# Kernel tuning notes

Measured on AMD Instinct MI355X. Metric: run time of the kernel, lower is better.

## Reference

```python
import jax, jax.numpy as jnp
import numpy as np

BS, SEQ, D = 8, 2048, 128
MASK_VALUE = -1000000.0


def setup_inputs() -> dict:
    key = jax.random.key(0)
    kq, kk, kv, kl = jax.random.split(key, 4)
    return {
        "queries": jax.random.normal(kq, (BS, SEQ, D), dtype=jnp.float32),
        "keys": jax.random.normal(kk, (BS, SEQ, D), dtype=jnp.float32),
        "values": jax.random.normal(kv, (BS, SEQ, D), dtype=jnp.float32),
        "valid_lens": jax.random.randint(kl, (BS,), 1, SEQ + 1, dtype=jnp.int32),
    }


def reference(queries, keys, values, valid_lens):
    d_k = keys.shape[-1]
    # (bs, seq_q, seq_k)
    scores = jnp.einsum("bqd,bkd->bqk", queries, keys) / jnp.sqrt(
        jnp.asarray(d_k, dtype=queries.dtype)
    )
    # padding mask over the LAST axis: position k valid iff k < valid_len[b]
    pos = jnp.arange(scores.shape[-1])  # (seq_k,)
    valid = pos[None, None, :] < valid_lens[:, None, None]  # (bs, 1, seq_k)
    scores = jnp.where(valid, scores, MASK_VALUE)
    attn = jax.nn.softmax(scores, axis=-1)
    # (bs, seq_q, d_v); dropout=0.0 -> identity
    return jnp.einsum("bqk,bkd->bqd", attn, values)
```

## Files before the change

### kernel.cpp

```cpp
#include <hip/hip_runtime.h>

typedef float f32x4 __attribute__((ext_vector_type(4)));
typedef short bf16x8 __attribute__((ext_vector_type(8)));
typedef short bf16x4 __attribute__((ext_vector_type(4)));
typedef unsigned int u32x2 __attribute__((ext_vector_type(2)));

#define BS    8
#define SEQ   2048
#define DH    128
#define BQ    32
#define BK    64
#define NT    256
#define CFIX  8.0f
#define SC2E  0.12751743f
#define NC2E  -11.541560327f

__device__ __forceinline__ unsigned short f2bf(float x) {
    unsigned u = __float_as_uint(x);
    u += 0x7FFFu + ((u >> 16) & 1u);
    return (unsigned short)(u >> 16);
}

__device__ __forceinline__ void gl_lds16(const unsigned short* g, unsigned short* l) {
    __builtin_amdgcn_global_load_lds(
        (const __attribute__((address_space(1))) unsigned int*)g,
        (__attribute__((address_space(3))) unsigned int*)l, 16, 0, 0);
}

__global__ __launch_bounds__(NT)
void conv_all(const float* __restrict__ K, const float* __restrict__ V,
              unsigned short* __restrict__ Kbf, unsigned short* __restrict__ Vt) {
    __shared__ unsigned short T[64][132];
    const int tid = threadIdx.x;
    const int bid = blockIdx.x;

    const int gtid = bid * NT + tid;
    #pragma unroll
    for (int i = 0; i < 8; ++i) {
        const int idx = i * (256 * NT) + gtid;
        float4 v = ((const float4*)K)[idx];
        ushort4 h;
        h.x = f2bf(v.x); h.y = f2bf(v.y); h.z = f2bf(v.z); h.w = f2bf(v.w);
        ((ushort4*)Kbf)[idx] = h;
    }

    const int vb = bid >> 5, s0 = (bid & 31) * 64;
    const float* Vb = V + ((size_t)vb * SEQ + s0) * DH;
    #pragma unroll
    for (int i = 0; i < 8; ++i) {
        const int row = i * 8 + (tid >> 5);
        const int col = (tid & 31) * 4;
        float4 v = *(const float4*)(Vb + (size_t)row * DH + col);
        ushort4 h;
        h.x = f2bf(v.x); h.y = f2bf(v.y); h.z = f2bf(v.z); h.w = f2bf(v.w);
        *(ushort4*)&T[row][col] = h;
    }
    __syncthreads();
    const int d = tid >> 1, sh = (tid & 1) * 32;
    unsigned short tmp[32] __attribute__((aligned(16)));
    #pragma unroll
    for (int s = 0; s < 32; ++s) tmp[s] = T[sh + s][d];
    unsigned short* dst = Vt + ((size_t)vb * DH + d) * SEQ + s0 + sh;
    #pragma unroll
    for (int g = 0; g < 4; ++g)
        *(uint4*)(dst + g * 8) = *(const uint4*)(tmp + g * 8);
}

__global__ __launch_bounds__(NT, 2)
void attn32sk(const float* __restrict__ Q, const unsigned short* __restrict__ Kbf,
              const unsigned short* __restrict__ Vt, const int* __restrict__ vlens,
              float* __restrict__ Oh, float* __restrict__ Lh) {
    __shared__ unsigned short Ks[2][BK * DH];
    __shared__ unsigned short Vs[2][DH * BK];
    __shared__ float Lsc[2][32];

    const int tid  = threadIdx.x;
    const int wid  = tid >> 6, lane = tid & 63;
    const int quad = lane >> 4, l16 = lane & 15;
    const int qh   = wid >> 1, sh = wid & 1;
    const int bid  = blockIdx.x;
    const int h    = bid & 1;
    const int rest = bid >> 1;
    const int b    = rest >> 6;
    const int q0   = (rest & 63) * BQ;
    const int vl   = vlens[b];

    const int ntiles = (vl + BK - 1) >> 6;
    const int t0 = h << 4;
    const int t1 = min(ntiles, (h + 1) << 4);

    float* Lrow = Lh + ((size_t)h * BS + b) * SEQ + q0;
    if (t0 >= t1) {
        if (tid < BQ) Lrow[tid] = 0.0f;
        return;
    }

    const unsigned short* Kb  = Kbf + (size_t)b * SEQ * DH;
    const unsigned short* Vtb = Vt  + (size_t)b * DH * SEQ;

    bf16x8 qf[4];
    {
        const float* Qr = Q + ((size_t)b * SEQ + q0 + 16 * qh + l16) * DH;
        #pragma unroll
        for (int ks = 0; ks < 4; ++ks) {
            const float4 x = *(const float4*)(Qr + 32 * ks + 8 * quad);
            const float4 y = *(const float4*)(Qr + 32 * ks + 8 * quad + 4);
            unsigned short t8[8] __attribute__((aligned(16)));
            t8[0] = f2bf(x.x); t8[1] = f2bf(x.y); t8[2] = f2bf(x.z); t8[3] = f2bf(x.w);
            t8[4] = f2bf(y.x); t8[5] = f2bf(y.y); t8[6] = f2bf(y.z); t8[7] = f2bf(y.w);
            qf[ks] = *(const bf16x8*)t8;
        }
    }

    f32x4 o[8];
    #pragma unroll
    for (int n = 0; n < 8; ++n) o[n] = (f32x4){0.f, 0.f, 0.f, 0.f};
    float lsum = 0.f;

    auto stage = [&](int buf, int k0) {
        unsigned short* KsB = &Ks[buf][0];
        unsigned short* VsB = &Vs[buf][0];
        #pragma unroll
        for (int ii = 0; ii < 4; ++ii) {
            const int rb = 16 * wid + 4 * ii;
            const int r  = rb + (lane >> 4);
            const int c  = lane & 15;
            gl_lds16(Kb + (size_t)(k0 + r) * DH + ((c ^ (r & 15)) << 3),
                     KsB + (size_t)rb * DH);
        }
        #pragma unroll
        for (int jj = 0; jj < 4; ++jj) {
            const int db = 32 * wid + 8 * jj;
            const int d  = db + (lane >> 3);
            const int c  = lane & 7;
            gl_lds16(Vtb + (size_t)d * SEQ + k0 + ((c ^ (d & 7)) << 3),
                     VsB + (size_t)db * BK);
        }
    };

    stage(0, t0 << 6);

    for (int t = t0; t < t1; ++t) {
        const int k0 = t << 6;
        __syncthreads();
        if (t + 1 < t1) stage((t + 1) & 1, k0 + BK);

        const unsigned short* Kt  = &Ks[t & 1][0];
        const unsigned short* Vtl = &Vs[t & 1][0];

        f32x4 s2[2];
        s2[0] = (f32x4){0.f, 0.f, 0.f, 0.f};
        s2[1] = (f32x4){0.f, 0.f, 0.f, 0.f};
        __builtin_amdgcn_s_setprio(1);
        #pragma unroll
        for (int ks = 0; ks < 4; ++ks) {
            bf16x8 bk[2];
            #pragma unroll
            for (int nt = 0; nt < 2; ++nt)
                bk[nt] = *(const bf16x8*)(Kt + (size_t)(32 * sh + 16 * nt + l16) * DH +
                                          (((4 * ks + quad) ^ l16) << 3));
            #pragma unroll
            for (int nt = 0; nt < 2; ++nt)
                s2[nt] = __builtin_amdgcn_mfma_f32_16x16x32_bf16(bk[nt], qf[ks], s2[nt], 0, 0, 0);
        }
        __builtin_amdgcn_s_setprio(0);

        float p[2][4];
        if (k0 + BK <= vl) {
            #pragma unroll
            for (int nt = 0; nt < 2; ++nt)
                #pragma unroll
                for (int r = 0; r < 4; ++r) {
                    const float pv = __builtin_amdgcn_exp2f(fmaf(s2[nt][r], SC2E, NC2E));
                    p[nt][r] = pv;
                    lsum += pv;
                }
        } else {
            const int kb = k0 + 32 * sh + 4 * quad;
            #pragma unroll
            for (int nt = 0; nt < 2; ++nt)
                #pragma unroll
                for (int r = 0; r < 4; ++r) {
                    float pv = __builtin_amdgcn_exp2f(fmaf(s2[nt][r], SC2E, NC2E));
                    pv = (kb + 16 * nt + r < vl) ? pv : 0.0f;
                    p[nt][r] = pv;
                    lsum += pv;
                }
        }

        bf16x4 pa[2];
        #pragma unroll
        for (int nt = 0; nt < 2; ++nt) {
            unsigned w0, w1;
            asm("v_cvt_pk_bf16_f32 %0, %1, %2" : "=v"(w0) : "v"(p[nt][0]), "v"(p[nt][1]));
            asm("v_cvt_pk_bf16_f32 %0, %1, %2" : "=v"(w1) : "v"(p[nt][2]), "v"(p[nt][3]));
            u32x2 tw; tw.x = w0; tw.y = w1;
            pa[nt] = __builtin_bit_cast(bf16x4, tw);
        }

        __builtin_amdgcn_s_setprio(1);
        #pragma unroll
        for (int n = 0; n < 8; ++n) {
            const int dd = 16 * n + l16;
            #pragma unroll
            for (int nt = 0; nt < 2; ++nt) {
                const int g = 4 * sh + 2 * nt + (quad >> 1);
                const bf16x4 vb = *(const bf16x4*)(Vtl + (size_t)dd * BK +
                                        ((g ^ (dd & 7)) << 3) + ((quad & 1) << 2));
                o[n] = __builtin_amdgcn_mfma_f32_16x16x16bf16_1k(pa[nt], vb, o[n], 0, 0, 0);
            }
        }
        __builtin_amdgcn_s_setprio(0);
    }

    lsum += __shfl_xor(lsum, 16, 64);
    lsum += __shfl_xor(lsum, 32, 64);

    __syncthreads();
    float* Osc = (float*)&Ks[0][0];

    if (lane < 16) Lsc[sh][qh * 16 + l16] = lsum;
    if (sh == 0) {
        #pragma unroll
        for (int r = 0; r < 4; ++r) {
            float* dst = Osc + (size_t)qh * 2048 + (4 * quad + r) * 128 + l16;
            #pragma unroll
            for (int n = 0; n < 8; ++n) dst[16 * n] = o[n][r];
        }
    }
    __syncthreads();
    if (sh == 1) {
        #pragma unroll
        for (int r = 0; r < 4; ++r) {
            const int row = 16 * qh + 4 * quad + r;
            const float ls = Lsc[0][qh * 16 + 4 * quad + r] +
                             Lsc[1][qh * 16 + 4 * quad + r];
            const float* src = Osc + (size_t)qh * 2048 + (4 * quad + r) * 128 + l16;
            float* Or = Oh + (((size_t)h * BS + b) * SEQ + q0 + row) * DH + l16;
            #pragma unroll
            for (int n = 0; n < 8; ++n)
                Or[16 * n] = o[n][r] + src[16 * n];
            if (l16 == 0) Lrow[row] = ls;
        }
    }
}

__global__ __launch_bounds__(NT)
void combine(const float* __restrict__ Oh, const float* __restrict__ Lh,
             float* __restrict__ Out) {
    const int bid = blockIdx.x;
    const int tid = threadIdx.x;
    const int b = bid >> 6, q0 = (bid & 63) * BQ;
    const int row = q0 + (tid >> 3);
    const int c0 = (tid & 7) * 16;
    const size_t r0 = (size_t)b * SEQ + row;

    const float l0 = Lh[r0];
    const float l1 = Lh[(size_t)BS * SEQ + r0];
    const float inv = 1.0f / (l0 + l1);

    const float* p0 = Oh + r0 * DH + c0;
    const float* p1 = Oh + (size_t)BS * SEQ * DH + r0 * DH + c0;
    float* po = Out + r0 * DH + c0;

    if (l1 != 0.0f) {
        #pragma unroll
        for (int j = 0; j < 4; ++j) {
            f32x4 a = *(const f32x4*)(p0 + 4 * j) + *(const f32x4*)(p1 + 4 * j);
            float4 ov;
            ov.x = a[0] * inv; ov.y = a[1] * inv;
            ov.z = a[2] * inv; ov.w = a[3] * inv;
            *(float4*)(po + 4 * j) = ov;
        }
    } else {
        #pragma unroll
        for (int j = 0; j < 4; ++j) {
            const f32x4 a = *(const f32x4*)(p0 + 4 * j);
            float4 ov;
            ov.x = a[0] * inv; ov.y = a[1] * inv;
            ov.z = a[2] * inv; ov.w = a[3] * inv;
            *(float4*)(po + 4 * j) = ov;
        }
    }
}

#define FBQ 32
#define QSTRIDE (DH + 4)
#define PSTRIDE (BK + 4)
__global__ __launch_bounds__(NT, 2)
void attn_fwd(const float* __restrict__ Q, const float* __restrict__ K,
              const float* __restrict__ V, const int* __restrict__ vlens,
              float* __restrict__ Out) {
    __shared__ float Qs[FBQ][QSTRIDE];
    __shared__ float KVs[BK][QSTRIDE];
    __shared__ float Ps[FBQ][PSTRIDE];
    __shared__ float l_s[FBQ];
    const int tid = threadIdx.x;
    const int b = blockIdx.y, q0 = blockIdx.x * FBQ;
    const int vl = vlens[b];
    const float scale = 0.088388347648318441f;
    const float* Qb = Q + ((size_t)b * SEQ + q0) * DH;
    const float* Kb = K + (size_t)b * SEQ * DH;
    const float* Vb = V + (size_t)b * SEQ * DH;
    {
        const int r = tid >> 5, c4 = (tid & 31) * 4;
        #pragma unroll
        for (int i = 0; i < 4; ++i)
            *(float4*)&Qs[i * 8 + r][c4] = *(const float4*)(Qb + (size_t)(i * 8 + r) * DH + c4);
    }
    const int sty = tid >> 4, stx = tid & 15;
    const int brow = tid >> 3, bpart = tid & 7;
    const int prg = tid >> 5, pcg = tid & 31;
    float lacc = 0.0f;
    float O[4][4];
    #pragma unroll
    for (int i = 0; i < 4; ++i)
        #pragma unroll
        for (int j = 0; j < 4; ++j) O[i][j] = 0.0f;
    const int ntiles = (vl + BK - 1) / BK;
    for (int t = 0; t < ntiles; ++t) {
        const int k0 = t * BK;
        __syncthreads();
        {
            const int r = tid >> 5, c4 = (tid & 31) * 4;
            #pragma unroll
            for (int i = 0; i < 8; ++i)
                *(float4*)&KVs[i * 8 + r][c4] = *(const float4*)(Kb + (size_t)(k0 + i * 8 + r) * DH + c4);
        }
        __syncthreads();
        float s0[4] = {0.f, 0.f, 0.f, 0.f}, s1[4] = {0.f, 0.f, 0.f, 0.f};
        #pragma unroll 2
        for (int d = 0; d < DH; d += 4) {
            const float4 qa = *(const float4*)&Qs[2 * sty][d];
            const float4 qb = *(const float4*)&Qs[2 * sty + 1][d];
            #pragma unroll
            for (int j = 0; j < 4; ++j) {
                const float4 kk = *(const float4*)&KVs[4 * stx + j][d];
                s0[j] += qa.x * kk.x + qa.y * kk.y + qa.z * kk.z + qa.w * kk.w;
                s1[j] += qb.x * kk.x + qb.y * kk.y + qb.z * kk.z + qb.w * kk.w;
            }
        }
        #pragma unroll
        for (int j = 0; j < 4; ++j) {
            const int kk = k0 + 4 * stx + j;
            const bool valid = kk < vl;
            Ps[2 * sty][4 * stx + j]     = valid ? __expf(s0[j] * scale - CFIX) : 0.f;
            Ps[2 * sty + 1][4 * stx + j] = valid ? __expf(s1[j] * scale - CFIX) : 0.f;
        }
        __syncthreads();
        {
            float ps = 0.f;
            #pragma unroll
            for (int i = 0; i < 8; ++i) ps += Ps[brow][bpart * 8 + i];
            #pragma unroll
            for (int off = 1; off < 8; off <<= 1) ps += __shfl_xor(ps, off, 64);
            if (bpart == 0) lacc += ps;
        }
        {
            const int r = tid >> 5, c4 = (tid & 31) * 4;
            float4 vreg[8];
            #pragma unroll
            for (int i = 0; i < 8; ++i)
                vreg[i] = *(const float4*)(Vb + (size_t)(k0 + i * 8 + r) * DH + c4);
            __syncthreads();
            #pragma unroll
            for (int i = 0; i < 8; ++i) *(float4*)&KVs[i * 8 + r][c4] = vreg[i];
        }
        __syncthreads();
        for (int k = 0; k < BK; k += 4) {
            float4 pr[4];
            #pragma unroll
            for (int i = 0; i < 4; ++i) pr[i] = *(const float4*)&Ps[prg * 4 + i][k];
            #pragma unroll
            for (int k2 = 0; k2 < 4; ++k2) {
                const float4 vv = *(const float4*)&KVs[k + k2][pcg * 4];
                #pragma unroll
                for (int i = 0; i < 4; ++i) {
                    const float p = ((const float*)&pr[i])[k2];
                    O[i][0] += p * vv.x; O[i][1] += p * vv.y;
                    O[i][2] += p * vv.z; O[i][3] += p * vv.w;
                }
            }
        }
    }
    if (bpart == 0) l_s[brow] = lacc;
    __syncthreads();
    float* Ob = Out + ((size_t)b * SEQ + q0) * DH;
    #pragma unroll
    for (int i = 0; i < 4; ++i) {
        const int row = prg * 4 + i;
        const float inv = 1.0f / l_s[row];
        float4 ov;
        ov.x = O[i][0] * inv; ov.y = O[i][1] * inv;
        ov.z = O[i][2] * inv; ov.w = O[i][3] * inv;
        *(float4*)(Ob + (size_t)row * DH + pcg * 4) = ov;
    }
}

extern "C" void kernel_launch(void* const* d_in, const int* in_sizes, int n_in,
                              void* d_out, int out_size, void* d_ws, size_t ws_size,
                              hipStream_t stream) {
    const float* Q = (const float*)d_in[0];
    const float* K = (const float*)d_in[1];
    const float* V = (const float*)d_in[2];
    const int* vlens = (const int*)d_in[3];
    float* Out = (float*)d_out;

    const size_t n = (size_t)BS * SEQ * DH;
    const size_t need = 2 * n * 2
                      + 2 * n * 4
                      + 2 * (size_t)BS * SEQ * 4;

    if (ws_size >= need) {
        unsigned short* Kbf = (unsigned short*)d_ws;
        unsigned short* Vt  = Kbf + n;
        float* Oh = (float*)(Vt + n);
        float* Lh = Oh + 2 * n;
        conv_all<<<dim3(256), dim3(NT), 0, stream>>>(K, V, Kbf, Vt);
        attn32sk<<<dim3(2 * BS * (SEQ / BQ)), dim3(NT), 0, stream>>>(Q, Kbf, Vt, vlens, Oh, Lh);
        combine<<<dim3(BS * (SEQ / BQ)), dim3(NT), 0, stream>>>(Oh, Lh, Out);
    } else {
        attn_fwd<<<dim3(SEQ / FBQ, BS), dim3(NT), 0, stream>>>(Q, K, V, vlens, Out);
    }
}
```

Baseline: 126.6 us.

## Use persistent attention kernel with atomic work queue, 64-row Q tiles, triple buffering

The split-K attention kernel becomes a persistent kernel: 256 blocks of 512 threads pull (half, batch, 64-query) work items from an atomic counter. The counter is reset in the conversion kernel, which now also converts Q to bf16. Each block covers 64 query rows with 8 waves, so every staged K/V tile is shared by twice as many queries. Loads use a three-stage LDS ring with explicit vmcnt waits instead of double buffering, meant to improve load balance across uneven valid lengths and to hide memory latency. The trade-offs are the extra Q conversion pass, the atomic overhead and more LDS per block, which may limit occupancy.

```diff
diff --git a/kernel.cpp b/kernel.cpp
--- a/kernel.cpp
+++ b/kernel.cpp
@@ -8,9 +8,11 @@
 #define BS    8
 #define SEQ   2048
 #define DH    128
-#define BQ    32
 #define BK    64
-#define NT    256
+#define CNT   256
+#define ANT   512
+#define QI    64
+#define NITEMS 512
 #define CFIX  8.0f
 #define SC2E  0.12751743f
 #define NC2E  -11.541560327f
@@ -27,21 +29,27 @@
         (__attribute__((address_space(3))) unsigned int*)l, 16, 0, 0);
 }
 
-__global__ __launch_bounds__(NT)
-void conv_all(const float* __restrict__ K, const float* __restrict__ V,
-              unsigned short* __restrict__ Kbf, unsigned short* __restrict__ Vt) {
+__global__ __launch_bounds__(CNT)
+void conv_all(const float* __restrict__ Q, const float* __restrict__ K,
+              const float* __restrict__ V,
+              unsigned short* __restrict__ Qbf, unsigned short* __restrict__ Kbf,
+              unsigned short* __restrict__ Vt, int* __restrict__ ctr) {
     __shared__ unsigned short T[64][132];
     const int tid = threadIdx.x;
     const int bid = blockIdx.x;
-
-    const int gtid = bid * NT + tid;
+    if (bid == 0 && tid == 0) *ctr = 0;
+
+    const int gtid = bid * CNT + tid;
     #pragma unroll
     for (int i = 0; i < 8; ++i) {
-        const int idx = i * (256 * NT) + gtid;
-        float4 v = ((const float4*)K)[idx];
-        ushort4 h;
-        h.x = f2bf(v.x); h.y = f2bf(v.y); h.z = f2bf(v.z); h.w = f2bf(v.w);
-        ((ushort4*)Kbf)[idx] = h;
+        const int idx = i * (256 * CNT) + gtid;
+        float4 k4 = ((const float4*)K)[idx];
+        float4 q4 = ((const float4*)Q)[idx];
+        ushort4 hk, hq;
+        hk.x = f2bf(k4.x); hk.y = f2bf(k4.y); hk.z = f2bf(k4.z); hk.w = f2bf(k4.w);
+        hq.x = f2bf(q4.x); hq.y = f2bf(q4.y); hq.z = f2bf(q4.z); hq.w = f2bf(q4.w);
+        ((ushort4*)Kbf)[idx] = hk;
+        ((ushort4*)Qbf)[idx] = hq;
     }
 
     const int vb = bid >> 5, s0 = (bid & 31) * 64;
@@ -66,191 +74,202 @@
         *(uint4*)(dst + g * 8) = *(const uint4*)(tmp + g * 8);
 }
 
-__global__ __launch_bounds__(NT, 2)
-void attn32sk(const float* __restrict__ Q, const unsigned short* __restrict__ Kbf,
-              const unsigned short* __restrict__ Vt, const int* __restrict__ vlens,
-              float* __restrict__ Oh, float* __restrict__ Lh) {
-    __shared__ unsigned short Ks[2][BK * DH];
-    __shared__ unsigned short Vs[2][DH * BK];
-    __shared__ float Lsc[2][32];
+__global__ __launch_bounds__(ANT, 2)
+void attn_q(const unsigned short* __restrict__ Qbf, const unsigned short* __restrict__ Kbf,
+            const unsigned short* __restrict__ Vt, const int* __restrict__ vlens,
+            float* __restrict__ Oh, float* __restrict__ Lh, int* __restrict__ ctr) {
+    __shared__ unsigned short KV[3 * 16384];
+    __shared__ int s_item;
 
     const int tid  = threadIdx.x;
     const int wid  = tid >> 6, lane = tid & 63;
     const int quad = lane >> 4, l16 = lane & 15;
     const int qh   = wid >> 1, sh = wid & 1;
-    const int bid  = blockIdx.x;
-    const int h    = bid & 1;
-    const int rest = bid >> 1;
-    const int b    = rest >> 6;
-    const int q0   = (rest & 63) * BQ;
-    const int vl   = vlens[b];
-
-    const int ntiles = (vl + BK - 1) >> 6;
-    const int t0 = h << 4;
-    const int t1 = min(ntiles, (h + 1) << 4);
-
-    float* Lrow = Lh + ((size_t)h * BS + b) * SEQ + q0;
-    if (t0 >= t1) {
-        if (tid < BQ) Lrow[tid] = 0.0f;
-        return;
-    }
-
-    const unsigned short* Kb  = Kbf + (size_t)b * SEQ * DH;
-    const unsigned short* Vtb = Vt  + (size_t)b * DH * SEQ;
-
-    bf16x8 qf[4];
-    {
-        const float* Qr = Q + ((size_t)b * SEQ + q0 + 16 * qh + l16) * DH;
-        #pragma unroll
-        for (int ks = 0; ks < 4; ++ks) {
-            const float4 x = *(const float4*)(Qr + 32 * ks + 8 * quad);
-            const float4 y = *(const float4*)(Qr + 32 * ks + 8 * quad + 4);
-            unsigned short t8[8] __attribute__((aligned(16)));
-            t8[0] = f2bf(x.x); t8[1] = f2bf(x.y); t8[2] = f2bf(x.z); t8[3] = f2bf(x.w);
-            t8[4] = f2bf(y.x); t8[5] = f2bf(y.y); t8[6] = f2bf(y.z); t8[7] = f2bf(y.w);
-            qf[ks] = *(const bf16x8*)t8;
-        }
-    }
-
-    f32x4 o[8];
-    #pragma unroll
-    for (int n = 0; n < 8; ++n) o[n] = (f32x4){0.f, 0.f, 0.f, 0.f};
-    float lsum = 0.f;
-
-    auto stage = [&](int buf, int k0) {
-        unsigned short* KsB = &Ks[buf][0];
-        unsigned short* VsB = &Vs[buf][0];
-        #pragma unroll
-        for (int ii = 0; ii < 4; ++ii) {
-            const int rb = 16 * wid + 4 * ii;
-            const int r  = rb + (lane >> 4);
-            const int c  = lane & 15;
-            gl_lds16(Kb + (size_t)(k0 + r) * DH + ((c ^ (r & 15)) << 3),
-                     KsB + (size_t)rb * DH);
-        }
-        #pragma unroll
-        for (int jj = 0; jj < 4; ++jj) {
-            const int db = 32 * wid + 8 * jj;
-            const int d  = db + (lane >> 3);
-            const int c  = lane & 7;
-            gl_lds16(Vtb + (size_t)d * SEQ + k0 + ((c ^ (d & 7)) << 3),
-                     VsB + (size_t)db * BK);
-        }
-    };
-
-    stage(0, t0 << 6);
-
-    for (int t = t0; t < t1; ++t) {
-        const int k0 = t << 6;
-        __syncthreads();
-        if (t + 1 < t1) stage((t + 1) & 1, k0 + BK);
-
-        const unsigned short* Kt  = &Ks[t & 1][0];
-        const unsigned short* Vtl = &Vs[t & 1][0];
-
-        f32x4 s2[2];
-        s2[0] = (f32x4){0.f, 0.f, 0.f, 0.f};
-        s2[1] = (f32x4){0.f, 0.f, 0.f, 0.f};
-        __builtin_amdgcn_s_setprio(1);
-        #pragma unroll
-        for (int ks = 0; ks < 4; ++ks) {
-            bf16x8 bk[2];
-            #pragma unroll
-            for (int nt = 0; nt < 2; ++nt)
-                bk[nt] = *(const bf16x8*)(Kt + (size_t)(32 * sh + 16 * nt + l16) * DH +
-                                          (((4 * ks + quad) ^ l16) << 3));
-            #pragma unroll
-            for (int nt = 0; nt < 2; ++nt)
-                s2[nt] = __builtin_amdgcn_mfma_f32_16x16x32_bf16(bk[nt], qf[ks], s2[nt], 0, 0, 0);
-        }
-        __builtin_amdgcn_s_setprio(0);
-
-        float p[2][4];
-        if (k0 + BK <= vl) {
-            #pragma unroll
-            for (int nt = 0; nt < 2; ++nt)
-                #pragma unroll
-                for (int r = 0; r < 4; ++r) {
-                    const float pv = __builtin_amdgcn_exp2f(fmaf(s2[nt][r], SC2E, NC2E));
-                    p[nt][r] = pv;
-                    lsum += pv;
+
+    for (;;) {
+        if (tid == 0) s_item = atomicAdd(ctr, 1);
+        __syncthreads();
+        const int it = s_item;
+        if (it >= NITEMS) break;
+
+        const int h  = it >> 8;
+        const int j  = it & 255;
+        const int b  = j & 7;
+        const int q0 = (j >> 3) * QI;
+        const int vl = vlens[b];
+        const int ntAll = (vl + BK - 1) >> 6;
+        const int t0 = h << 4;
+        const int t1 = min(ntAll, (h + 1) << 4);
+        float* Lrow = Lh + ((size_t)h * BS + b) * SEQ + q0;
+
+        if (t0 >= t1) {
+            if (tid < QI) Lrow[tid] = 0.0f;
+            __syncthreads();
+            continue;
+        }
+        const int nt = t1 - t0;
+
+        const unsigned short* Kb  = Kbf + (size_t)b * SEQ * DH;
+        const unsigned short* Vtb = Vt  + (size_t)b * DH * SEQ;
+
+        auto stage = [&](int buf, int k0) {
+            unsigned short* KsB = &KV[buf * 16384];
+            unsigned short* VsB = KsB + 8192;
+            #pragma unroll
+            for (int ii = 0; ii < 2; ++ii) {
+                const int rb = 8 * wid + 4 * ii;
+                const int r  = rb + (lane >> 4);
+                const int c  = lane & 15;
+                gl_lds16(Kb + (size_t)(k0 + r) * DH + ((c ^ (r & 15)) << 3),
+                         KsB + (size_t)rb * DH);
+            }
+            #pragma unroll
+            for (int jj = 0; jj < 2; ++jj) {
+                const int db = 16 * wid + 8 * jj;
+                const int d  = db + (lane >> 3);
+                const int c  = lane & 7;
+                gl_lds16(Vtb + (size_t)d * SEQ + k0 + ((c ^ (d & 7)) << 3),
+                         VsB + (size_t)db * BK);
+            }
+        };
+
+        int issued = 1, sbuf = 1;
+        stage(0, t0 << 6);
+        if (nt > 1) { stage(1, (t0 + 1) << 6); issued = 2; sbuf = 2; }
+
+        bf16x8 qf[4];
+        {
+            const unsigned short* Qr = Qbf + ((size_t)b * SEQ + q0 + 16 * qh + l16) * DH;
+            #pragma unroll
+            for (int ks = 0; ks < 4; ++ks)
+                qf[ks] = *(const bf16x8*)(Qr + 32 * ks + 8 * quad);
+        }
+
+        f32x4 o[8];
+        #pragma unroll
+        for (int n = 0; n < 8; ++n) o[n] = (f32x4){0.f, 0.f, 0.f, 0.f};
+        float lsum = 0.f;
+        int cbuf = 0;
+
+        for (int tt = 0; tt < nt; ++tt) {
+            if (issued > tt + 1) asm volatile("s_waitcnt vmcnt(4)" ::: "memory");
+            else                 asm volatile("s_waitcnt vmcnt(0)" ::: "memory");
+            __builtin_amdgcn_s_barrier();
+            if (issued < nt) {
+                stage(sbuf, (t0 + issued) << 6);
+                ++issued;
+                sbuf = (sbuf == 2) ? 0 : sbuf + 1;
+            }
+
+            const unsigned short* Kt  = &KV[cbuf * 16384];
+            const unsigned short* Vtl = Kt + 8192;
+            const int k0 = (t0 + tt) << 6;
+
+            f32x4 s2[2];
+            s2[0] = (f32x4){0.f, 0.f, 0.f, 0.f};
+            s2[1] = (f32x4){0.f, 0.f, 0.f, 0.f};
+            __builtin_amdgcn_s_setprio(1);
+            #pragma unroll
+            for (int ks = 0; ks < 4; ++ks) {
+                bf16x8 bk[2];
+                #pragma unroll
+                for (int g = 0; g < 2; ++g)
+                    bk[g] = *(const bf16x8*)(Kt + (size_t)(32 * sh + 16 * g + l16) * DH +
+                                             (((4 * ks + quad) ^ l16) << 3));
+                #pragma unroll
+                for (int g = 0; g < 2; ++g)
+                    s2[g] = __builtin_amdgcn_mfma_f32_16x16x32_bf16(bk[g], qf[ks], s2[g], 0, 0, 0);
+            }
+            __builtin_amdgcn_s_setprio(0);
+
+            float p[2][4];
+            if (k0 + BK <= vl) {
+                #pragma unroll
+                for (int g = 0; g < 2; ++g)
+                    #pragma unroll
+                    for (int r = 0; r < 4; ++r) {
+                        const float pv = __builtin_amdgcn_exp2f(fmaf(s2[g][r], SC2E, NC2E));
+                        p[g][r] = pv;
+                        lsum += pv;
+                    }
+            } else {
+                const int kb = k0 + 32 * sh + 4 * quad;
+                #pragma unroll
+                for (int g = 0; g < 2; ++g)
+                    #pragma unroll
+                    for (int r = 0; r < 4; ++r) {
+                        float pv = __builtin_amdgcn_exp2f(fmaf(s2[g][r], SC2E, NC2E));
+                        pv = (kb + 16 * g + r < vl) ? pv : 0.0f;
+                        p[g][r] = pv;
+                        lsum += pv;
+                    }
+            }
+
+            bf16x4 pa[2];
+            #pragma unroll
+            for (int g = 0; g < 2; ++g) {
+                unsigned w0, w1;
+                asm("v_cvt_pk_bf16_f32 %0, %1, %2" : "=v"(w0) : "v"(p[g][0]), "v"(p[g][1]));
+                asm("v_cvt_pk_bf16_f32 %0, %1, %2" : "=v"(w1) : "v"(p[g][2]), "v"(p[g][3]));
+                u32x2 tw; tw.x = w0; tw.y = w1;
+                pa[g] = __builtin_bit_cast(bf16x4, tw);
+            }
+
+            __builtin_amdgcn_s_setprio(1);
+            #pragma unroll
+            for (int n = 0; n < 8; ++n) {
+                const int dd = 16 * n + l16;
+                #pragma unroll
+                for (int g = 0; g < 2; ++g) {
+                    const int gc = 4 * sh + 2 * g + (quad >> 1);
+                    const bf16x4 vb = *(const bf16x4*)(Vtl + (size_t)dd * BK +
+                                            ((gc ^ (dd & 7)) << 3) + ((quad & 1) << 2));
+                    o[n] = __builtin_amdgcn_mfma_f32_16x16x16bf16_1k(pa[g], vb, o[n], 0, 0, 0);
                 }
-        } else {
-            const int kb = k0 + 32 * sh + 4 * quad;
-            #pragma unroll
-            for (int nt = 0; nt < 2; ++nt)
-                #pragma unroll
-                for (int r = 0; r < 4; ++r) {
-                    float pv = __builtin_amdgcn_exp2f(fmaf(s2[nt][r], SC2E, NC2E));
-                    pv = (kb + 16 * nt + r < vl) ? pv : 0.0f;
-                    p[nt][r] = pv;
-                    lsum += pv;
-                }
-        }
-
-        bf16x4 pa[2];
-        #pragma unroll
-        for (int nt = 0; nt < 2; ++nt) {
-            unsigned w0, w1;
-            asm("v_cvt_pk_bf16_f32 %0, %1, %2" : "=v"(w0) : "v"(p[nt][0]), "v"(p[nt][1]));
-            asm("v_cvt_pk_bf16_f32 %0, %1, %2" : "=v"(w1) : "v"(p[nt][2]), "v"(p[nt][3]));
-            u32x2 tw; tw.x = w0; tw.y = w1;
-            pa[nt] = __builtin_bit_cast(bf16x4, tw);
-        }
-
-        __builtin_amdgcn_s_setprio(1);
-        #pragma unroll
-        for (int n = 0; n < 8; ++n) {
-            const int dd = 16 * n + l16;
-            #pragma unroll
-            for (int nt = 0; nt < 2; ++nt) {
-                const int g = 4 * sh + 2 * nt + (quad >> 1);
-                const bf16x4 vb = *(const bf16x4*)(Vtl + (size_t)dd * BK +
-                                        ((g ^ (dd & 7)) << 3) + ((quad & 1) << 2));
-                o[n] = __builtin_amdgcn_mfma_f32_16x16x16bf16_1k(pa[nt], vb, o[n], 0, 0, 0);
-            }
-        }
-        __builtin_amdgcn_s_setprio(0);
-    }
-
-    lsum += __shfl_xor(lsum, 16, 64);
-    lsum += __shfl_xor(lsum, 32, 64);
-
-    __syncthreads();
-    float* Osc = (float*)&Ks[0][0];
-
-    if (lane < 16) Lsc[sh][qh * 16 + l16] = lsum;
-    if (sh == 0) {
-        #pragma unroll
-        for (int r = 0; r < 4; ++r) {
-            float* dst = Osc + (size_t)qh * 2048 + (4 * quad + r) * 128 + l16;
-            #pragma unroll
-            for (int n = 0; n < 8; ++n) dst[16 * n] = o[n][r];
-        }
-    }
-    __syncthreads();
-    if (sh == 1) {
-        #pragma unroll
-        for (int r = 0; r < 4; ++r) {
-            const int row = 16 * qh + 4 * quad + r;
-            const float ls = Lsc[0][qh * 16 + 4 * quad + r] +
-                             Lsc[1][qh * 16 + 4 * quad + r];
-            const float* src = Osc + (size_t)qh * 2048 + (4 * quad + r) * 128 + l16;
-            float* Or = Oh + (((size_t)h * BS + b) * SEQ + q0 + row) * DH + l16;
-            #pragma unroll
-            for (int n = 0; n < 8; ++n)
-                Or[16 * n] = o[n][r] + src[16 * n];
-            if (l16 == 0) Lrow[row] = ls;
-        }
-    }
-}
-
-__global__ __launch_bounds__(NT)
+            }
+            __builtin_amdgcn_s_setprio(0);
+            cbuf = (cbuf == 2) ? 0 : cbuf + 1;
+        }
+
+        lsum += __shfl_xor(lsum, 16, 64);
+        lsum += __shfl_xor(lsum, 32, 64);
+
+        __syncthreads();
+        float* Osc = (float*)&KV[0];
+        float* Lsc = Osc + 8192;
+
+        if (lane < 16) Lsc[sh * 64 + 16 * qh + l16] = lsum;
+        if (sh == 0) {
+            #pragma unroll
+            for (int r = 0; r < 4; ++r) {
+                float* dst = Osc + (size_t)qh * 2048 + (4 * quad + r) * 128 + l16;
+                #pragma unroll
+                for (int n = 0; n < 8; ++n) dst[16 * n] = o[n][r];
+            }
+        }
+        __syncthreads();
+        if (sh == 1) {
+            #pragma unroll
+            for (int r = 0; r < 4; ++r) {
+                const int row = 16 * qh + 4 * quad + r;
+                const float ls = Lsc[row] + Lsc[64 + row];
+                const float* src = Osc + (size_t)qh * 2048 + (4 * quad + r) * 128 + l16;
+                float* Or = Oh + (((size_t)h * BS + b) * SEQ + q0 + row) * DH + l16;
+                #pragma unroll
+                for (int n = 0; n < 8; ++n)
+                    Or[16 * n] = o[n][r] + src[16 * n];
+                if (l16 == 0) Lrow[row] = ls;
+            }
+        }
+    }
+}
+
+__global__ __launch_bounds__(CNT)
 void combine(const float* __restrict__ Oh, const float* __restrict__ Lh,
              float* __restrict__ Out) {
     const int bid = blockIdx.x;
     const int tid = threadIdx.x;
-    const int b = bid >> 6, q0 = (bid & 63) * BQ;
+    const int b = bid >> 6, q0 = (bid & 63) * 32;
     const int row = q0 + (tid >> 3);
     const int c0 = (tid & 7) * 16;
     const size_t r0 = (size_t)b * SEQ + row;
@@ -265,21 +284,21 @@
 
     if (l1 != 0.0f) {
         #pragma unroll
-        for (int j = 0; j < 4; ++j) {
-            f32x4 a = *(const f32x4*)(p0 + 4 * j) + *(const f32x4*)(p1 + 4 * j);
+        for (int jj = 0; jj < 4; ++jj) {
+            f32x4 a = *(const f32x4*)(p0 + 4 * jj) + *(const f32x4*)(p1 + 4 * jj);
             float4 ov;
             ov.x = a[0] * inv; ov.y = a[1] * inv;
             ov.z = a[2] * inv; ov.w = a[3] * inv;
-            *(float4*)(po + 4 * j) = ov;
+            *(float4*)(po + 4 * jj) = ov;
         }
     } else {
         #pragma unroll
-        for (int j = 0; j < 4; ++j) {
-            const f32x4 a = *(const f32x4*)(p0 + 4 * j);
+        for (int jj = 0; jj < 4; ++jj) {
+            const f32x4 a = *(const f32x4*)(p0 + 4 * jj);
             float4 ov;
             ov.x = a[0] * inv; ov.y = a[1] * inv;
             ov.z = a[2] * inv; ov.w = a[3] * inv;
-            *(float4*)(po + 4 * j) = ov;
+            *(float4*)(po + 4 * jj) = ov;
         }
     }
 }
@@ -287,7 +306,7 @@
 #define FBQ 32
 #define QSTRIDE (DH + 4)
 #define PSTRIDE (BK + 4)
-__global__ __launch_bounds__(NT, 2)
+__global__ __launch_bounds__(CNT, 2)
 void attn_fwd(const float* __restrict__ Q, const float* __restrict__ K,
               const float* __restrict__ V, const int* __restrict__ vlens,
               float* __restrict__ Out) {
@@ -316,7 +335,7 @@
     #pragma unroll
     for (int i = 0; i < 4; ++i)
         #pragma unroll
-        for (int j = 0; j < 4; ++j) O[i][j] = 0.0f;
+        for (int jj = 0; jj < 4; ++jj) O[i][jj] = 0.0f;
     const int ntiles = (vl + BK - 1) / BK;
     for (int t = 0; t < ntiles; ++t) {
         const int k0 = t * BK;
@@ -334,18 +353,18 @@
             const float4 qa = *(const float4*)&Qs[2 * sty][d];
             const float4 qb = *(const float4*)&Qs[2 * sty + 1][d];
             #pragma unroll
-            for (int j = 0; j < 4; ++j) {
-                const float4 kk = *(const float4*)&KVs[4 * stx + j][d];
-                s0[j] += qa.x * kk.x + qa.y * kk.y + qa.z * kk.z + qa.w * kk.w;
-                s1[j] += qb.x * kk.x + qb.y * kk.y + qb.z * kk.z + qb.w * kk.w;
-            }
-        }
-        #pragma unroll
-        for (int j = 0; j < 4; ++j) {
-            const int kk = k0 + 4 * stx + j;
+            for (int jj = 0; jj < 4; ++jj) {
+                const float4 kk = *(const float4*)&KVs[4 * stx + jj][d];
+                s0[jj] += qa.x * kk.x + qa.y * kk.y + qa.z * kk.z + qa.w * kk.w;
+                s1[jj] += qb.x * kk.x + qb.y * kk.y + qb.z * kk.z + qb.w * kk.w;
+            }
+        }
+        #pragma unroll
+        for (int jj = 0; jj < 4; ++jj) {
+            const int kk = k0 + 4 * stx + jj;
             const bool valid = kk < vl;
-            Ps[2 * sty][4 * stx + j]     = valid ? __expf(s0[j] * scale - CFIX) : 0.f;
-            Ps[2 * sty + 1][4 * stx + j] = valid ? __expf(s1[j] * scale - CFIX) : 0.f;
+            Ps[2 * sty][4 * stx + jj]     = valid ? __expf(s0[jj] * scale - CFIX) : 0.f;
+            Ps[2 * sty + 1][4 * stx + jj] = valid ? __expf(s1[jj] * scale - CFIX) : 0.f;
         }
         __syncthreads();
         {
@@ -407,19 +426,22 @@
     float* Out = (float*)d_out;
 
     const size_t n = (size_t)BS * SEQ * DH;
-    const size_t need = 2 * n * 2
+    const size_t need = 3 * n * 2
                       + 2 * n * 4
-                      + 2 * (size_t)BS * SEQ * 4;
+                      + 2 * (size_t)BS * SEQ * 4
+                      + 64;
 
     if (ws_size >= need) {
         unsigned short* Kbf = (unsigned short*)d_ws;
         unsigned short* Vt  = Kbf + n;
-        float* Oh = (float*)(Vt + n);
+        unsigned short* Qbf = Vt + n;
+        float* Oh = (float*)(Qbf + n);
         float* Lh = Oh + 2 * n;
-        conv_all<<<dim3(256), dim3(NT), 0, stream>>>(K, V, Kbf, Vt);
-        attn32sk<<<dim3(2 * BS * (SEQ / BQ)), dim3(NT), 0, stream>>>(Q, Kbf, Vt, vlens, Oh, Lh);
-        combine<<<dim3(BS * (SEQ / BQ)), dim3(NT), 0, stream>>>(Oh, Lh, Out);
+        int* ctr  = (int*)(Lh + 2 * (size_t)BS * SEQ);
+        conv_all<<<dim3(256), dim3(CNT), 0, stream>>>(Q, K, V, Qbf, Kbf, Vt, ctr);
+        attn_q<<<dim3(256), dim3(ANT), 0, stream>>>(Qbf, Kbf, Vt, vlens, Oh, Lh, ctr);
+        combine<<<dim3(BS * (SEQ / 32)), dim3(CNT), 0, stream>>>(Oh, Lh, Out);
     } else {
-        attn_fwd<<<dim3(SEQ / FBQ, BS), dim3(NT), 0, stream>>>(Q, K, V, vlens, Out);
-    }
-}
+        attn_fwd<<<dim3(SEQ / FBQ, BS), dim3(CNT), 0, stream>>>(Q, K, V, vlens, Out);
+    }
+}
```

Result: faster. 123.2 us (-2.6%).

## Process 64 query rows per block to reuse staged K/V tiles twice

Applied to the files above, without the earlier changes.

Doubles the query tile per block from 32 to 64 rows. Each wave now holds two query groups, so every K and V fragment read from LDS feeds two MFMAs instead of one. The goal is to halve K/V global-to-LDS staging and LDS reads per query row, at the cost of twice the accumulator registers and half as many blocks in the grid. The combine kernel and the fallback path are adjusted to keep their old 32-row and 64-key tiling.

```diff
diff --git a/kernel.cpp b/kernel.cpp
--- a/kernel.cpp
+++ b/kernel.cpp
@@ -8,7 +8,7 @@
 #define BS    8
 #define SEQ   2048
 #define DH    128
-#define BQ    32
+#define BQ    64
 #define BK    64
 #define NT    256
 #define CFIX  8.0f
@@ -67,12 +67,12 @@
 }
 
 __global__ __launch_bounds__(NT, 2)
-void attn32sk(const float* __restrict__ Q, const unsigned short* __restrict__ Kbf,
+void attn64sk(const float* __restrict__ Q, const unsigned short* __restrict__ Kbf,
               const unsigned short* __restrict__ Vt, const int* __restrict__ vlens,
               float* __restrict__ Oh, float* __restrict__ Lh) {
     __shared__ unsigned short Ks[2][BK * DH];
     __shared__ unsigned short Vs[2][DH * BK];
-    __shared__ float Lsc[2][32];
+    __shared__ float Lsc[2][64];
 
     const int tid  = threadIdx.x;
     const int wid  = tid >> 6, lane = tid & 63;
@@ -81,13 +81,13 @@
     const int bid  = blockIdx.x;
     const int h    = bid & 1;
     const int rest = bid >> 1;
-    const int b    = rest >> 6;
-    const int q0   = (rest & 63) * BQ;
+    const int b    = rest >> 5;
+    const int q0   = (rest & 31) * BQ;
     const int vl   = vlens[b];
 
-    const int ntiles = (vl + BK - 1) >> 6;
+    const int ntAll = (vl + BK - 1) >> 6;
     const int t0 = h << 4;
-    const int t1 = min(ntiles, (h + 1) << 4);
+    const int t1 = min(ntAll, (h + 1) << 4);
 
     float* Lrow = Lh + ((size_t)h * BS + b) * SEQ + q0;
     if (t0 >= t1) {
@@ -98,9 +98,10 @@
     const unsigned short* Kb  = Kbf + (size_t)b * SEQ * DH;
     const unsigned short* Vtb = Vt  + (size_t)b * DH * SEQ;
 
-    bf16x8 qf[4];
-    {
-        const float* Qr = Q + ((size_t)b * SEQ + q0 + 16 * qh + l16) * DH;
+    bf16x8 qf[2][4];
+    #pragma unroll
+    for (int qg = 0; qg < 2; ++qg) {
+        const float* Qr = Q + ((size_t)b * SEQ + q0 + 32 * qg + 16 * qh + l16) * DH;
         #pragma unroll
         for (int ks = 0; ks < 4; ++ks) {
             const float4 x = *(const float4*)(Qr + 32 * ks + 8 * quad);
@@ -108,14 +109,16 @@
             unsigned short t8[8] __attribute__((aligned(16)));
             t8[0] = f2bf(x.x); t8[1] = f2bf(x.y); t8[2] = f2bf(x.z); t8[3] = f2bf(x.w);
             t8[4] = f2bf(y.x); t8[5] = f2bf(y.y); t8[6] = f2bf(y.z); t8[7] = f2bf(y.w);
-            qf[ks] = *(const bf16x8*)t8;
-        }
-    }
-
-    f32x4 o[8];
-    #pragma unroll
-    for (int n = 0; n < 8; ++n) o[n] = (f32x4){0.f, 0.f, 0.f, 0.f};
-    float lsum = 0.f;
+            qf[qg][ks] = *(const bf16x8*)t8;
+        }
+    }
+
+    f32x4 o[2][8];
+    #pragma unroll
+    for (int qg = 0; qg < 2; ++qg)
+        #pragma unroll
+        for (int n = 0; n < 8; ++n) o[qg][n] = (f32x4){0.f, 0.f, 0.f, 0.f};
+    float lsum[2] = {0.f, 0.f};
 
     auto stage = [&](int buf, int k0) {
         unsigned short* KsB = &Ks[buf][0];
@@ -148,9 +151,12 @@
         const unsigned short* Kt  = &Ks[t & 1][0];
         const unsigned short* Vtl = &Vs[t & 1][0];
 
-        f32x4 s2[2];
-        s2[0] = (f32x4){0.f, 0.f, 0.f, 0.f};
-        s2[1] = (f32x4){0.f, 0.f, 0.f, 0.f};
+        f32x4 s2[2][2];
+        #pragma unroll
+        for (int qg = 0; qg < 2; ++qg) {
+            s2[qg][0] = (f32x4){0.f, 0.f, 0.f, 0.f};
+            s2[qg][1] = (f32x4){0.f, 0.f, 0.f, 0.f};
+        }
         __builtin_amdgcn_s_setprio(1);
         #pragma unroll
         for (int ks = 0; ks < 4; ++ks) {
@@ -161,42 +167,51 @@
                                           (((4 * ks + quad) ^ l16) << 3));
             #pragma unroll
             for (int nt = 0; nt < 2; ++nt)
-                s2[nt] = __builtin_amdgcn_mfma_f32_16x16x32_bf16(bk[nt], qf[ks], s2[nt], 0, 0, 0);
+                #pragma unroll
+                for (int qg = 0; qg < 2; ++qg)
+                    s2[qg][nt] = __builtin_amdgcn_mfma_f32_16x16x32_bf16(
+                        bk[nt], qf[qg][ks], s2[qg][nt], 0, 0, 0);
         }
         __builtin_amdgcn_s_setprio(0);
 
-        float p[2][4];
+        float p[2][2][4];
         if (k0 + BK <= vl) {
             #pragma unroll
-            for (int nt = 0; nt < 2; ++nt)
-                #pragma unroll
-                for (int r = 0; r < 4; ++r) {
-                    const float pv = __builtin_amdgcn_exp2f(fmaf(s2[nt][r], SC2E, NC2E));
-                    p[nt][r] = pv;
-                    lsum += pv;
-                }
+            for (int qg = 0; qg < 2; ++qg)
+                #pragma unroll
+                for (int nt = 0; nt < 2; ++nt)
+                    #pragma unroll
+                    for (int r = 0; r < 4; ++r) {
+                        const float pv = __builtin_amdgcn_exp2f(fmaf(s2[qg][nt][r], SC2E, NC2E));
+                        p[qg][nt][r] = pv;
+                        lsum[qg] += pv;
+                    }
         } else {
             const int kb = k0 + 32 * sh + 4 * quad;
             #pragma unroll
-            for (int nt = 0; nt < 2; ++nt)
-                #pragma unroll
-                for (int r = 0; r < 4; ++r) {
-                    float pv = __builtin_amdgcn_exp2f(fmaf(s2[nt][r], SC2E, NC2E));
-                    pv = (kb + 16 * nt + r < vl) ? pv : 0.0f;
-                    p[nt][r] = pv;
-                    lsum += pv;
-                }
-        }
-
-        bf16x4 pa[2];
-        #pragma unroll
-        for (int nt = 0; nt < 2; ++nt) {
-            unsigned w0, w1;
-            asm("v_cvt_pk_bf16_f32 %0, %1, %2" : "=v"(w0) : "v"(p[nt][0]), "v"(p[nt][1]));
-            asm("v_cvt_pk_bf16_f32 %0, %1, %2" : "=v"(w1) : "v"(p[nt][2]), "v"(p[nt][3]));
-            u32x2 tw; tw.x = w0; tw.y = w1;
-            pa[nt] = __builtin_bit_cast(bf16x4, tw);
-        }
+            for (int qg = 0; qg < 2; ++qg)
+                #pragma unroll
+                for (int nt = 0; nt < 2; ++nt)
+                    #pragma unroll
+                    for (int r = 0; r < 4; ++r) {
+                        float pv = __builtin_amdgcn_exp2f(fmaf(s2[qg][nt][r], SC2E, NC2E));
+                        pv = (kb + 16 * nt + r < vl) ? pv : 0.0f;
+                        p[qg][nt][r] = pv;
+                        lsum[qg] += pv;
+                    }
+        }
+
+        bf16x4 pa[2][2];
+        #pragma unroll
+        for (int qg = 0; qg < 2; ++qg)
+            #pragma unroll
+            for (int nt = 0; nt < 2; ++nt) {
+                unsigned w0, w1;
+                asm("v_cvt_pk_bf16_f32 %0, %1, %2" : "=v"(w0) : "v"(p[qg][nt][0]), "v"(p[qg][nt][1]));
+                asm("v_cvt_pk_bf16_f32 %0, %1, %2" : "=v"(w1) : "v"(p[qg][nt][2]), "v"(p[qg][nt][3]));
+                u32x2 tw; tw.x = w0; tw.y = w1;
+                pa[qg][nt] = __builtin_bit_cast(bf16x4, tw);
+            }
 
         __builtin_amdgcn_s_setprio(1);
         #pragma unroll
@@ -207,41 +222,56 @@
                 const int g = 4 * sh + 2 * nt + (quad >> 1);
                 const bf16x4 vb = *(const bf16x4*)(Vtl + (size_t)dd * BK +
                                         ((g ^ (dd & 7)) << 3) + ((quad & 1) << 2));
-                o[n] = __builtin_amdgcn_mfma_f32_16x16x16bf16_1k(pa[nt], vb, o[n], 0, 0, 0);
+                #pragma unroll
+                for (int qg = 0; qg < 2; ++qg)
+                    o[qg][n] = __builtin_amdgcn_mfma_f32_16x16x16bf16_1k(
+                        pa[qg][nt], vb, o[qg][n], 0, 0, 0);
             }
         }
         __builtin_amdgcn_s_setprio(0);
     }
 
-    lsum += __shfl_xor(lsum, 16, 64);
-    lsum += __shfl_xor(lsum, 32, 64);
+    #pragma unroll
+    for (int qg = 0; qg < 2; ++qg) {
+        lsum[qg] += __shfl_xor(lsum[qg], 16, 64);
+        lsum[qg] += __shfl_xor(lsum[qg], 32, 64);
+    }
 
     __syncthreads();
     float* Osc = (float*)&Ks[0][0];
 
-    if (lane < 16) Lsc[sh][qh * 16 + l16] = lsum;
+    if (lane < 16) {
+        Lsc[sh][qh * 16 + l16]      = lsum[0];
+        Lsc[sh][32 + qh * 16 + l16] = lsum[1];
+    }
     if (sh == 0) {
         #pragma unroll
-        for (int r = 0; r < 4; ++r) {
-            float* dst = Osc + (size_t)qh * 2048 + (4 * quad + r) * 128 + l16;
-            #pragma unroll
-            for (int n = 0; n < 8; ++n) dst[16 * n] = o[n][r];
-        }
+        for (int qg = 0; qg < 2; ++qg)
+            #pragma unroll
+            for (int r = 0; r < 4; ++r) {
+                float* dst = Osc + (size_t)qg * 4096 + (size_t)qh * 2048 +
+                             (4 * quad + r) * 128 + l16;
+                #pragma unroll
+                for (int n = 0; n < 8; ++n) dst[16 * n] = o[qg][n][r];
+            }
     }
     __syncthreads();
     if (sh == 1) {
         #pragma unroll
-        for (int r = 0; r < 4; ++r) {
-            const int row = 16 * qh + 4 * quad + r;
-            const float ls = Lsc[0][qh * 16 + 4 * quad + r] +
-                             Lsc[1][qh * 16 + 4 * quad + r];
-            const float* src = Osc + (size_t)qh * 2048 + (4 * quad + r) * 128 + l16;
-            float* Or = Oh + (((size_t)h * BS + b) * SEQ + q0 + row) * DH + l16;
-            #pragma unroll
-            for (int n = 0; n < 8; ++n)
-                Or[16 * n] = o[n][r] + src[16 * n];
-            if (l16 == 0) Lrow[row] = ls;
-        }
+        for (int qg = 0; qg < 2; ++qg)
+            #pragma unroll
+            for (int r = 0; r < 4; ++r) {
+                const int rloc = qh * 16 + 4 * quad + r;
+                const int row  = 32 * qg + rloc;
+                const float ls = Lsc[0][32 * qg + rloc] + Lsc[1][32 * qg + rloc];
+                const float* src = Osc + (size_t)qg * 4096 + (size_t)qh * 2048 +
+                                   (4 * quad + r) * 128 + l16;
+                float* Or = Oh + (((size_t)h * BS + b) * SEQ + q0 + row) * DH + l16;
+                #pragma unroll
+                for (int n = 0; n < 8; ++n)
+                    Or[16 * n] = o[qg][n][r] + src[16 * n];
+                if (l16 == 0) Lrow[row] = ls;
+            }
     }
 }
 
@@ -250,7 +280,7 @@
              float* __restrict__ Out) {
     const int bid = blockIdx.x;
     const int tid = threadIdx.x;
-    const int b = bid >> 6, q0 = (bid & 63) * BQ;
+    const int b = bid >> 6, q0 = (bid & 63) * 32;
     const int row = q0 + (tid >> 3);
     const int c0 = (tid & 7) * 16;
     const size_t r0 = (size_t)b * SEQ + row;
@@ -285,14 +315,15 @@
 }
 
 #define FBQ 32
+#define FBK 64
 #define QSTRIDE (DH + 4)
-#define PSTRIDE (BK + 4)
+#define PSTRIDE (FBK + 4)
 __global__ __launch_bounds__(NT, 2)
 void attn_fwd(const float* __restrict__ Q, const float* __restrict__ K,
               const float* __restrict__ V, const int* __restrict__ vlens,
               float* __restrict__ Out) {
     __shared__ float Qs[FBQ][QSTRIDE];
-    __shared__ float KVs[BK][QSTRIDE];
+    __shared__ float KVs[FBK][QSTRIDE];
     __shared__ float Ps[FBQ][PSTRIDE];
     __shared__ float l_s[FBQ];
     const int tid = threadIdx.x;
@@ -316,10 +347,10 @@
     #pragma unroll
     for (int i = 0; i < 4; ++i)
         #pragma unroll
-        for (int j = 0; j < 4; ++j) O[i][j] = 0.0f;
-    const int ntiles = (vl + BK - 1) / BK;
+        for (int jj = 0; jj < 4; ++jj) O[i][jj] = 0.0f;
+    const int ntiles = (vl + FBK - 1) / FBK;
     for (int t = 0; t < ntiles; ++t) {
-        const int k0 = t * BK;
+        const int k0 = t * FBK;
         __syncthreads();
         {
             const int r = tid >> 5, c4 = (tid & 31) * 4;
@@ -334,18 +365,18 @@
             const float4 qa = *(const float4*)&Qs[2 * sty][d];
             const float4 qb = *(const float4*)&Qs[2 * sty + 1][d];
             #pragma unroll
-            for (int j = 0; j < 4; ++j) {
-                const float4 kk = *(const float4*)&KVs[4 * stx + j][d];
-                s0[j] += qa.x * kk.x + qa.y * kk.y + qa.z * kk.z + qa.w * kk.w;
-                s1[j] += qb.x * kk.x + qb.y * kk.y + qb.z * kk.z + qb.w * kk.w;
-            }
-        }
-        #pragma unroll
-        for (int j = 0; j < 4; ++j) {
-            const int kk = k0 + 4 * stx + j;
+            for (int jj = 0; jj < 4; ++jj) {
+                const float4 kk = *(const float4*)&KVs[4 * stx + jj][d];
+                s0[jj] += qa.x * kk.x + qa.y * kk.y + qa.z * kk.z + qa.w * kk.w;
+                s1[jj] += qb.x * kk.x + qb.y * kk.y + qb.z * kk.z + qb.w * kk.w;
+            }
+        }
+        #pragma unroll
+        for (int jj = 0; jj < 4; ++jj) {
+            const int kk = k0 + 4 * stx + jj;
             const bool valid = kk < vl;
-            Ps[2 * sty][4 * stx + j]     = valid ? __expf(s0[j] * scale - CFIX) : 0.f;
-            Ps[2 * sty + 1][4 * stx + j] = valid ? __expf(s1[j] * scale - CFIX) : 0.f;
+            Ps[2 * sty][4 * stx + jj]     = valid ? __expf(s0[jj] * scale - CFIX) : 0.f;
+            Ps[2 * sty + 1][4 * stx + jj] = valid ? __expf(s1[jj] * scale - CFIX) : 0.f;
         }
         __syncthreads();
         {
@@ -367,7 +398,7 @@
             for (int i = 0; i < 8; ++i) *(float4*)&KVs[i * 8 + r][c4] = vreg[i];
         }
         __syncthreads();
-        for (int k = 0; k < BK; k += 4) {
+        for (int k = 0; k < FBK; k += 4) {
             float4 pr[4];
             #pragma unroll
             for (int i = 0; i < 4; ++i) pr[i] = *(const float4*)&Ps[prg * 4 + i][k];
@@ -417,8 +448,8 @@
         float* Oh = (float*)(Vt + n);
         float* Lh = Oh + 2 * n;
         conv_all<<<dim3(256), dim3(NT), 0, stream>>>(K, V, Kbf, Vt);
-        attn32sk<<<dim3(2 * BS * (SEQ / BQ)), dim3(NT), 0, stream>>>(Q, Kbf, Vt, vlens, Oh, Lh);
-        combine<<<dim3(BS * (SEQ / BQ)), dim3(NT), 0, stream>>>(Oh, Lh, Out);
+        attn64sk<<<dim3(2 * BS * (SEQ / BQ)), dim3(NT), 0, stream>>>(Q, Kbf, Vt, vlens, Oh, Lh);
+        combine<<<dim3(BS * (SEQ / 32)), dim3(NT), 0, stream>>>(Oh, Lh, Out);
     } else {
         attn_fwd<<<dim3(SEQ / FBQ, BS), dim3(NT), 0, stream>>>(Q, K, V, vlens, Out);
     }
```

After: 111.1 us, median of 2. 1.14x faster.
